# Optimization experiments

Hardware: AMD Instinct MI355X
Metric: run time of the kernel (lower is better)

Reference implementation:

```python
import jax, jax.numpy as jnp
import numpy as np

B, S, D, H = 2, 2048, 2048, 16
HD = D // H  # 128


def setup_inputs() -> dict:
    key = jax.random.key(0)
    ks = jax.random.split(key, 9)
    s = 1.0 / np.sqrt(D)
    return {
        "x": jax.random.normal(ks[0], (B, S, D), dtype=jnp.float32),
        "Wq_w": jax.random.uniform(ks[1], (D, D), jnp.float32, -s, s),
        "Wq_b": jax.random.uniform(ks[2], (D,), jnp.float32, -s, s),
        "Wk_w": jax.random.uniform(ks[3], (HD, D), jnp.float32, -s, s),
        "Wk_b": jax.random.uniform(ks[4], (HD,), jnp.float32, -s, s),
        "Wv_w": jax.random.uniform(ks[5], (HD, D), jnp.float32, -s, s),
        "Wv_b": jax.random.uniform(ks[6], (HD,), jnp.float32, -s, s),
        "Wo_w": jax.random.uniform(ks[7], (D, D), jnp.float32, -s, s),
        "Wo_b": jax.random.uniform(ks[8], (D,), jnp.float32, -s, s),
    }


def reference(x, Wq_w, Wq_b, Wk_w, Wk_b, Wv_w, Wv_b, Wo_w, Wo_b):
    b, s, d = x.shape
    h, hd = H, HD
    # projections (torch Linear: x @ W.T + b)
    q = (x @ Wq_w.T + Wq_b).reshape(b, s, h, hd).transpose(0, 2, 1, 3)  # (b,h,s,hd)
    k = x @ Wk_w.T + Wk_b  # (b,s,hd) single shared KV head
    v = x @ Wv_w.T + Wv_b  # (b,s,hd)
    scores = jnp.einsum("bhsd,btd->bhst", q, k) / jnp.sqrt(jnp.float32(hd))
    attn = jax.nn.softmax(scores, axis=-1)
    out = jnp.einsum("bhst,btd->bhsd", attn, v)  # (b,h,s,hd)
    # faithful to original: reshape WITHOUT transposing heads back
    out = out.reshape(b, s, d)
    return out @ Wo_w.T + Wo_b
```

## Files before the change

### kernel.cpp

```cpp
#include <hip/hip_runtime.h>
#include <stdint.h>

#define BATCH 2
#define SEQ   2048
#define DMOD  2048
#define NHEAD 16
#define HDIM  128

typedef __bf16 bf16x8 __attribute__((ext_vector_type(8)));
typedef float f32x4   __attribute__((ext_vector_type(4)));
typedef float f32x16  __attribute__((ext_vector_type(16)));
typedef unsigned short u16x8 __attribute__((ext_vector_type(8)));

#define MFMA16(a, b, c) __builtin_amdgcn_mfma_f32_16x16x32_bf16(a, b, c, 0, 0, 0)
#define MFMA32(a, b, c) __builtin_amdgcn_mfma_f32_32x32x16_bf16(a, b, c, 0, 0, 0)

__device__ __forceinline__ uint16_t f2bf(float f) {
  union { float f; uint32_t u; } cv; cv.f = f;
  uint32_t u = cv.u;
  return (uint16_t)((u + 0x7FFFu + ((u >> 16) & 1u)) >> 16);
}

__device__ __forceinline__ float fexp2(float x) { return exp2f(x); }

__device__ __forceinline__ uint32_t pkbf(float a, float b) {
  uint32_t d;
  asm("v_cvt_pk_bf16_f32 %0, %1, %2" : "=v"(d) : "v"(a), "v"(b));
  return d;
}

__device__ __forceinline__ void gload_lds16(const void* g, void* l) {
  __builtin_amdgcn_global_load_lds(
      (__attribute__((address_space(1))) void*)g,
      (__attribute__((address_space(3))) void*)l, 16, 0, 0);
}

__global__ __launch_bounds__(256) void cvtbf16(const float* __restrict__ in,
                                               uint16_t* __restrict__ out, int n) {
  int i = (blockIdx.x * 256 + threadIdx.x) * 8;
  if (i >= n) return;
  f32x4 a = *(const f32x4*)&in[i];
  f32x4 b = *(const f32x4*)&in[i + 4];
  u16x8 o;
  o[0] = f2bf(a[0]); o[1] = f2bf(a[1]); o[2] = f2bf(a[2]); o[3] = f2bf(a[3]);
  o[4] = f2bf(b[0]); o[5] = f2bf(b[1]); o[6] = f2bf(b[2]); o[7] = f2bf(b[3]);
  *(u16x8*)&out[i] = o;
}

template <bool OUT_F32>
__device__ __forceinline__ void gemm128_body(
    const uint16_t* __restrict__ A, int lda,
    const uint16_t* __restrict__ Bw,
    const float* __restrict__ bias,
    void* __restrict__ out, int ldc,
    int m0, int n0, int K, float oscale,
    uint16_t* As, uint16_t* Bs) {
  const int t = threadIdx.x;
  const int lane = t & 63;
  const int w = t >> 6;
  const int half = lane >> 4;
  const int fr = lane & 15;
  const int wr = w >> 1, wc = w & 1;

  f32x4 acc[4][4] = {};

  const int r0 = (0 * 4 + w) * 16 + (lane >> 2);
  const int r1 = (1 * 4 + w) * 16 + (lane >> 2);
  const int sc0 = (lane & 3) * 8;

  const int nkt = K >> 5;
  for (int kt = 0; kt < nkt; ++kt) {
    const int kb = kt * 32;
    gload_lds16(&A[(size_t)(m0 + r0) * lda + kb + sc0], &As[(0 * 4 + w) * 512]);
    gload_lds16(&A[(size_t)(m0 + r1) * lda + kb + sc0], &As[(1 * 4 + w) * 512]);
    gload_lds16(&Bw[(size_t)(n0 + r0) * K + kb + sc0], &Bs[(0 * 4 + w) * 512]);
    gload_lds16(&Bw[(size_t)(n0 + r1) * K + kb + sc0], &Bs[(1 * 4 + w) * 512]);
    __syncthreads();
    bf16x8 af[4], bf[4];
#pragma unroll
    for (int i = 0; i < 4; ++i) {
      af[i] = *(const bf16x8*)&As[(wr * 64 + i * 16 + fr) * 32 + half * 8];
      bf[i] = *(const bf16x8*)&Bs[(wc * 64 + i * 16 + fr) * 32 + half * 8];
    }
#pragma unroll
    for (int i = 0; i < 4; ++i)
#pragma unroll
      for (int j = 0; j < 4; ++j)
        acc[i][j] = MFMA16(af[i], bf[j], acc[i][j]);
    __syncthreads();
  }

#pragma unroll
  for (int j = 0; j < 4; ++j) {
    const int col = wc * 64 + j * 16 + fr;
    const float bv = bias[n0 + col];
#pragma unroll
    for (int i = 0; i < 4; ++i) {
      const int rowb = m0 + wr * 64 + i * 16 + half * 4;
#pragma unroll
      for (int r = 0; r < 4; ++r) {
        const float v = (acc[i][j][r] + bv) * oscale;
        if (OUT_F32)
          ((float*)out)[(size_t)(rowb + r) * ldc + n0 + col] = v;
        else
          ((uint16_t*)out)[(size_t)(rowb + r) * ldc + n0 + col] = f2bf(v);
      }
    }
  }
}

__global__ __launch_bounds__(256, 2) void qkv_gemm(
    const uint16_t* __restrict__ xb,
    const uint16_t* __restrict__ wqb, const float* __restrict__ bq,
    const uint16_t* __restrict__ wkb, const float* __restrict__ bk,
    const uint16_t* __restrict__ wvb, const float* __restrict__ bv,
    uint16_t* __restrict__ qb, uint16_t* __restrict__ kb, uint16_t* __restrict__ vb,
    float qscale) {
  __shared__ uint16_t As[128 * 32];
  __shared__ uint16_t Bs[128 * 32];
  const int m0 = blockIdx.x * 128;
  const int y = blockIdx.y;
  const uint16_t* Bw;
  const float* bias;
  uint16_t* out;
  int n0, ldc;
  float os = 1.0f;
  if (y < 16)       { Bw = wqb; bias = bq; out = qb; n0 = y * 128; ldc = DMOD; os = qscale; }
  else if (y == 16) { Bw = wkb; bias = bk; out = kb; n0 = 0;       ldc = HDIM; }
  else              { Bw = wvb; bias = bv; out = vb; n0 = 0;       ldc = HDIM; }
  gemm128_body<false>(xb, DMOD, Bw, bias, out, ldc, m0, n0, DMOD, os, As, Bs);
}

__global__ __launch_bounds__(256, 2) void o_gemm(
    const uint16_t* __restrict__ ab, const uint16_t* __restrict__ wob,
    const float* __restrict__ bo, float* __restrict__ out) {
  __shared__ uint16_t As[128 * 32];
  __shared__ uint16_t Bs[128 * 32];
  gemm128_body<true>(ab, DMOD, wob, bo, out, DMOD,
                     blockIdx.x * 128, blockIdx.y * 128, DMOD, 1.0f, As, Bs);
}

__global__ __launch_bounds__(256) void transpose_v(const uint16_t* __restrict__ vb,
                                                   uint16_t* __restrict__ vt) {
  __shared__ uint16_t tile[64][65];
  const int s0 = blockIdx.x * 64, d0 = blockIdx.y * 64, b = blockIdx.z;
  const int tx = threadIdx.x & 63, ty = threadIdx.x >> 6;
#pragma unroll
  for (int r = ty; r < 64; r += 4)
    tile[r][tx] = vb[((size_t)b * SEQ + s0 + r) * HDIM + d0 + tx];
  __syncthreads();
#pragma unroll
  for (int r = ty; r < 64; r += 4)
    vt[((size_t)b * HDIM + d0 + r) * SEQ + s0 + tx] = tile[tx][r];
}

__global__ __launch_bounds__(256, 2) void mqa_attn(
    const uint16_t* __restrict__ qb,
    const uint16_t* __restrict__ kb,
    const uint16_t* __restrict__ vt,
    uint16_t* __restrict__ ab) {
  __shared__ uint16_t Ks[2][64 * 128];
  __shared__ uint16_t Vs[2][128 * 64];

  const int t = threadIdx.x, lane = t & 63, w = t >> 6;
  const int l31 = lane & 31, hi = lane >> 5;
  const int qt = blockIdx.x, h = blockIdx.y, b = blockIdx.z;
  const size_t rowbase = (size_t)b * SEQ;
  const int q0 = qt * 128 + w * 32;

  bf16x8 qf[8];
  {
    const uint16_t* qrow = &qb[(rowbase + q0 + l31) * DMOD + h * HDIM + hi * 8];
#pragma unroll
    for (int c8 = 0; c8 < 8; ++c8)
      qf[c8] = *(const bf16x8*)&qrow[c8 * 16];
  }

  f32x16 ot[4] = {};
  float lsum = 0.f;

  const int skrow = lane >> 4;
  const int skcol = (lane & 15) * 8;
  const int svrow = lane >> 3;
  const int svcol = (lane & 7) * 8;

#pragma unroll
  for (int c = 0; c < 4; ++c) {
    const int ch = c * 4 + w;
    const int krow = ch * 4 + skrow;
    gload_lds16(&kb[(rowbase + krow) * HDIM + (skcol ^ ((krow & 7) << 3))],
                &Ks[0][ch * 512]);
    const int vrow = ch * 8 + svrow;
    gload_lds16(&vt[((size_t)b * HDIM + vrow) * SEQ + (svcol ^ ((vrow & 7) << 3))],
                &Vs[0][ch * 512]);
  }
  __syncthreads();

  for (int kt = 0; kt < SEQ / 64; ++kt) {
    const int cur = kt & 1;
    if (kt < SEQ / 64 - 1) {
#pragma unroll
      for (int c = 0; c < 4; ++c) {
        const int ch = c * 4 + w;
        const int krow = ch * 4 + skrow;
        gload_lds16(&kb[(rowbase + (kt + 1) * 64 + krow) * HDIM +
                        (skcol ^ ((krow & 7) << 3))],
                    &Ks[cur ^ 1][ch * 512]);
        const int vrow = ch * 8 + svrow;
        gload_lds16(&vt[((size_t)b * HDIM + vrow) * SEQ + (kt + 1) * 64 +
                        (svcol ^ ((vrow & 7) << 3))],
                    &Vs[cur ^ 1][ch * 512]);
      }
    }

    f32x16 st[2] = {};
    __builtin_amdgcn_s_setprio(1);
#pragma unroll
    for (int c8 = 0; c8 < 8; ++c8) {
#pragma unroll
      for (int tt = 0; tt < 2; ++tt) {
        const int krow = tt * 32 + l31;
        bf16x8 kf = *(const bf16x8*)&Ks[cur][krow * 128 +
                        ((c8 * 16 + hi * 8) ^ ((krow & 7) << 3))];
        st[tt] = MFMA32(kf, qf[c8], st[tt]);
      }
    }
    __builtin_amdgcn_s_setprio(0);

    uint32_t wk[2][8], rk[2][8];
    float s = 0.f;
#pragma unroll
    for (int tt = 0; tt < 2; ++tt) {
      float e[16];
#pragma unroll
      for (int i = 0; i < 16; ++i) {
        e[i] = fexp2(st[tt][i]);
        s += e[i];
      }
#pragma unroll
      for (int i = 0; i < 8; ++i)
        wk[tt][i] = pkbf(e[2 * i], e[2 * i + 1]);
    }
    s += __shfl_xor(s, 32);
    lsum += s;

#pragma unroll
    for (int tt = 0; tt < 2; ++tt)
#pragma unroll
      for (int i = 0; i < 8; ++i)
        rk[tt][i] = (uint32_t)__shfl_xor((int)wk[tt][i], 32);

    bf16x8 pf[4];
#pragma unroll
    for (int tt = 0; tt < 2; ++tt) {
      union { uint32_t u[4]; bf16x8 v; } p0, p1;
      p0.u[0] = hi ? rk[tt][2] : wk[tt][0];
      p0.u[1] = hi ? rk[tt][3] : wk[tt][1];
      p0.u[2] = hi ? wk[tt][2] : rk[tt][0];
      p0.u[3] = hi ? wk[tt][3] : rk[tt][1];
      p1.u[0] = hi ? rk[tt][6] : wk[tt][4];
      p1.u[1] = hi ? rk[tt][7] : wk[tt][5];
      p1.u[2] = hi ? wk[tt][6] : rk[tt][4];
      p1.u[3] = hi ? wk[tt][7] : rk[tt][5];
      pf[2 * tt] = p0.v;
      pf[2 * tt + 1] = p1.v;
    }

    __builtin_amdgcn_s_setprio(1);
#pragma unroll
    for (int kc = 0; kc < 4; ++kc) {
#pragma unroll
      for (int dt = 0; dt < 4; ++dt) {
        const int vrow = dt * 32 + l31;
        bf16x8 vf = *(const bf16x8*)&Vs[cur][vrow * 64 +
                        ((kc * 16 + hi * 8) ^ ((vrow & 7) << 3))];
        ot[dt] = MFMA32(vf, pf[kc], ot[dt]);
      }
    }
    __builtin_amdgcn_s_setprio(0);

    __syncthreads();
  }

  const float inv = 1.f / lsum;
  const size_t orow = ((size_t)(b * NHEAD + h) * SEQ + q0 + l31) * HDIM;
#pragma unroll
  for (int dt = 0; dt < 4; ++dt)
#pragma unroll
    for (int qd = 0; qd < 4; ++qd) {
      ushort4 hv;
      hv.x = f2bf(ot[dt][qd * 4 + 0] * inv);
      hv.y = f2bf(ot[dt][qd * 4 + 1] * inv);
      hv.z = f2bf(ot[dt][qd * 4 + 2] * inv);
      hv.w = f2bf(ot[dt][qd * 4 + 3] * inv);
      *(ushort4*)&ab[orow + dt * 32 + qd * 8 + hi * 4] = hv;
    }
}

extern "C" void kernel_launch(void* const* d_in, const int* in_sizes, int n_in,
                              void* d_out, int out_size, void* d_ws, size_t ws_size,
                              hipStream_t stream) {
  const float* x    = (const float*)d_in[0];
  const float* Wq_w = (const float*)d_in[1];
  const float* Wq_b = (const float*)d_in[2];
  const float* Wk_w = (const float*)d_in[3];
  const float* Wk_b = (const float*)d_in[4];
  const float* Wv_w = (const float*)d_in[5];
  const float* Wv_b = (const float*)d_in[6];
  const float* Wo_w = (const float*)d_in[7];
  const float* Wo_b = (const float*)d_in[8];
  float* out = (float*)d_out;

  char* ws = (char*)d_ws;
  uint16_t* xb  = (uint16_t*)(ws + 0);
  uint16_t* ab  = xb;
  uint16_t* wqb = (uint16_t*)(ws + 16777216);
  uint16_t* vt  = wqb;
  uint16_t* wkb = (uint16_t*)(ws + 25165824);
  uint16_t* wvb = (uint16_t*)(ws + 25690112);
  uint16_t* wob = (uint16_t*)(ws + 26214400);
  uint16_t* qb  = (uint16_t*)(ws + 34603008);
  uint16_t* kb  = (uint16_t*)(ws + 51380224);
  uint16_t* vb  = (uint16_t*)(ws + 52428800);

  const float qscale = 0.08838834764831845f * 1.4426950408889634f;

  cvtbf16<<<4096, 256, 0, stream>>>(x, xb, BATCH * SEQ * DMOD);
  cvtbf16<<<2048, 256, 0, stream>>>(Wq_w, wqb, DMOD * DMOD);
  cvtbf16<<<128, 256, 0, stream>>>(Wk_w, wkb, HDIM * DMOD);
  cvtbf16<<<128, 256, 0, stream>>>(Wv_w, wvb, HDIM * DMOD);
  cvtbf16<<<2048, 256, 0, stream>>>(Wo_w, wob, DMOD * DMOD);

  qkv_gemm<<<dim3(32, 18), 256, 0, stream>>>(xb, wqb, Wq_b, wkb, Wk_b, wvb, Wv_b,
                                             qb, kb, vb, qscale);
  transpose_v<<<dim3(32, 2, 2), 256, 0, stream>>>(vb, vt);
  mqa_attn<<<dim3(16, 16, 2), 256, 0, stream>>>(qb, kb, vt, ab);
  o_gemm<<<dim3(32, 16), 256, 0, stream>>>(ab, wob, Wo_b, out);
}
```

Measured before the change: 309.0 us.

## Rewrite GEMMs as 128x256 triple-buffered 8-wave kernel; use permlane32 swap in attention

Replaces the 128x128, single-stage GEMM with a 512-thread kernel that computes 128x256 tiles with K=64 steps. Loads are triple-buffered into swizzled LDS and overlapped with MFMA using explicit vmcnt waits, and tiles are mapped to XCDs for L2 locality. K and V projections are fused into one 256-wide tile alongside the Q tiles. In attention, the bf16 probability exchange between wave halves uses v_permlane32_swap instead of 16 shuffles plus selects. The larger dynamic LDS and one block per CU lower occupancy, so latency hiding relies on the pipeline.

Measured after the change: 317.2 us. +2.6%, slower.

```diff
diff --git a/kernel.cpp b/kernel.cpp
--- a/kernel.cpp
+++ b/kernel.cpp
@@ -47,97 +47,120 @@
   *(u16x8*)&out[i] = o;
 }
 
-template <bool OUT_F32>
-__device__ __forceinline__ void gemm128_body(
-    const uint16_t* __restrict__ A, int lda,
-    const uint16_t* __restrict__ Bw,
-    const float* __restrict__ bias,
-    void* __restrict__ out, int ldc,
-    int m0, int n0, int K, float oscale,
-    uint16_t* As, uint16_t* Bs) {
-  const int t = threadIdx.x;
-  const int lane = t & 63;
-  const int w = t >> 6;
-  const int half = lane >> 4;
-  const int fr = lane & 15;
-  const int wr = w >> 1, wc = w & 1;
+template <bool OUT_F32, bool HAS_KV>
+__global__ __launch_bounds__(512, 1) void gemm8(
+    const uint16_t* __restrict__ A,
+    const uint16_t* __restrict__ Bw, const float* __restrict__ bias,
+    void* __restrict__ out, int ldc, float oscale,
+    const uint16_t* __restrict__ Bkv,
+    const float* __restrict__ biask, const float* __restrict__ biasv,
+    uint16_t* __restrict__ kout, uint16_t* __restrict__ vout) {
+  extern __shared__ uint16_t smem[];
+  uint16_t* As = smem;
+  uint16_t* Bs = smem + 3 * 128 * 64;
+
+  const int lane = threadIdx.x & 63, w = threadIdx.x >> 6;
+  const int half = lane >> 4, fr = lane & 15;
+  const int wr = w >> 2, wc = w & 3;
+
+  const int f = blockIdx.x;
+  bool kvblk = false;
+  int m0, n0;
+  const uint16_t* Bb;
+  if (HAS_KV && f >= 256) {
+    kvblk = true; m0 = (f - 256) * 128; n0 = 0; Bb = Bkv;
+  } else {
+    const int xcd = f & 7, idx = f >> 3;
+    const int mblk = (xcd >> 1) * 8 + (idx & 7);
+    const int nblk = (xcd & 1) * 4 + (idx >> 3);
+    m0 = mblk * 128; n0 = nblk * 256; Bb = Bw;
+  }
+
+  const int rsub = lane >> 3;
+  const int swcol = ((lane & 7) ^ rsub) * 8;
+  const size_t a0 = (size_t)(m0 + (2 * w) * 8 + rsub) * DMOD + swcol;
+  const size_t b0 = (size_t)(n0 + (4 * w) * 8 + rsub) * DMOD + swcol;
 
   f32x4 acc[4][4] = {};
-
-  const int r0 = (0 * 4 + w) * 16 + (lane >> 2);
-  const int r1 = (1 * 4 + w) * 16 + (lane >> 2);
-  const int sc0 = (lane & 3) * 8;
-
-  const int nkt = K >> 5;
-  for (int kt = 0; kt < nkt; ++kt) {
-    const int kb = kt * 32;
-    gload_lds16(&A[(size_t)(m0 + r0) * lda + kb + sc0], &As[(0 * 4 + w) * 512]);
-    gload_lds16(&A[(size_t)(m0 + r1) * lda + kb + sc0], &As[(1 * 4 + w) * 512]);
-    gload_lds16(&Bw[(size_t)(n0 + r0) * K + kb + sc0], &Bs[(0 * 4 + w) * 512]);
-    gload_lds16(&Bw[(size_t)(n0 + r1) * K + kb + sc0], &Bs[(1 * 4 + w) * 512]);
-    __syncthreads();
-    bf16x8 af[4], bf[4];
-#pragma unroll
-    for (int i = 0; i < 4; ++i) {
-      af[i] = *(const bf16x8*)&As[(wr * 64 + i * 16 + fr) * 32 + half * 8];
-      bf[i] = *(const bf16x8*)&Bs[(wc * 64 + i * 16 + fr) * 32 + half * 8];
-    }
-#pragma unroll
-    for (int i = 0; i < 4; ++i)
+  const int NT = DMOD / 64;
+
+  auto STAGE = [&](int kt, int slot) {
+    uint16_t* Ad = As + slot * (128 * 64);
+    uint16_t* Bd = Bs + slot * (256 * 64);
+    const int kk = kt * 64;
+    gload_lds16(&A[a0 + kk],            &Ad[(2 * w) * 512]);
+    gload_lds16(&A[a0 + 8 * DMOD + kk], &Ad[(2 * w + 1) * 512]);
+    gload_lds16(&Bb[b0 + kk],             &Bd[(4 * w) * 512]);
+    gload_lds16(&Bb[b0 + 8 * DMOD + kk],  &Bd[(4 * w + 1) * 512]);
+    gload_lds16(&Bb[b0 + 16 * DMOD + kk], &Bd[(4 * w + 2) * 512]);
+    gload_lds16(&Bb[b0 + 24 * DMOD + kk], &Bd[(4 * w + 3) * 512]);
+  };
+
+  STAGE(0, 0);
+  STAGE(1, 1);
+  asm volatile("s_waitcnt vmcnt(6)" ::: "memory");
+  __builtin_amdgcn_s_barrier();
+  asm volatile("" ::: "memory");
+
+  int sc_ = 0, ss_ = 2;
+#pragma unroll 1
+  for (int t = 0; t < NT; ++t) {
+    if (t + 2 < NT) STAGE(t + 2, ss_);
+
+    const uint16_t* Ar = As + sc_ * (128 * 64);
+    const uint16_t* Br = Bs + sc_ * (256 * 64);
+#pragma unroll
+    for (int kc = 0; kc < 2; ++kc) {
+      bf16x8 af[4], bf[4];
+      const int slot = ((kc * 4 + half) ^ (fr & 7)) * 8;
+#pragma unroll
+      for (int i = 0; i < 4; ++i)
+        af[i] = *(const bf16x8*)&Ar[(wr * 64 + i * 16 + fr) * 64 + slot];
 #pragma unroll
       for (int j = 0; j < 4; ++j)
-        acc[i][j] = MFMA16(af[i], bf[j], acc[i][j]);
-    __syncthreads();
-  }
-
+        bf[j] = *(const bf16x8*)&Br[(wc * 64 + j * 16 + fr) * 64 + slot];
+      __builtin_amdgcn_s_setprio(1);
+#pragma unroll
+      for (int i = 0; i < 4; ++i)
+#pragma unroll
+        for (int j = 0; j < 4; ++j)
+          acc[i][j] = MFMA16(af[i], bf[j], acc[i][j]);
+      __builtin_amdgcn_s_setprio(0);
+    }
+
+    if (t + 2 < NT) asm volatile("s_waitcnt vmcnt(6)" ::: "memory");
+    else            asm volatile("s_waitcnt vmcnt(0)" ::: "memory");
+    if (t + 1 < NT) {
+      __builtin_amdgcn_s_barrier();
+      asm volatile("" ::: "memory");
+    }
+    sc_ = (sc_ == 2) ? 0 : sc_ + 1;
+    ss_ = (ss_ == 2) ? 0 : ss_ + 1;
+  }
+
+  const float os = kvblk ? 1.0f : oscale;
 #pragma unroll
   for (int j = 0; j < 4; ++j) {
     const int col = wc * 64 + j * 16 + fr;
-    const float bv = bias[n0 + col];
+    float bv_;
+    if (!kvblk) bv_ = bias[n0 + col];
+    else        bv_ = (col < 128) ? biask[col] : biasv[col - 128];
 #pragma unroll
     for (int i = 0; i < 4; ++i) {
       const int rowb = m0 + wr * 64 + i * 16 + half * 4;
 #pragma unroll
       for (int r = 0; r < 4; ++r) {
-        const float v = (acc[i][j][r] + bv) * oscale;
-        if (OUT_F32)
-          ((float*)out)[(size_t)(rowb + r) * ldc + n0 + col] = v;
-        else
-          ((uint16_t*)out)[(size_t)(rowb + r) * ldc + n0 + col] = f2bf(v);
-      }
-    }
-  }
-}
-
-__global__ __launch_bounds__(256, 2) void qkv_gemm(
-    const uint16_t* __restrict__ xb,
-    const uint16_t* __restrict__ wqb, const float* __restrict__ bq,
-    const uint16_t* __restrict__ wkb, const float* __restrict__ bk,
-    const uint16_t* __restrict__ wvb, const float* __restrict__ bv,
-    uint16_t* __restrict__ qb, uint16_t* __restrict__ kb, uint16_t* __restrict__ vb,
-    float qscale) {
-  __shared__ uint16_t As[128 * 32];
-  __shared__ uint16_t Bs[128 * 32];
-  const int m0 = blockIdx.x * 128;
-  const int y = blockIdx.y;
-  const uint16_t* Bw;
-  const float* bias;
-  uint16_t* out;
-  int n0, ldc;
-  float os = 1.0f;
-  if (y < 16)       { Bw = wqb; bias = bq; out = qb; n0 = y * 128; ldc = DMOD; os = qscale; }
-  else if (y == 16) { Bw = wkb; bias = bk; out = kb; n0 = 0;       ldc = HDIM; }
-  else              { Bw = wvb; bias = bv; out = vb; n0 = 0;       ldc = HDIM; }
-  gemm128_body<false>(xb, DMOD, Bw, bias, out, ldc, m0, n0, DMOD, os, As, Bs);
-}
-
-__global__ __launch_bounds__(256, 2) void o_gemm(
-    const uint16_t* __restrict__ ab, const uint16_t* __restrict__ wob,
-    const float* __restrict__ bo, float* __restrict__ out) {
-  __shared__ uint16_t As[128 * 32];
-  __shared__ uint16_t Bs[128 * 32];
-  gemm128_body<true>(ab, DMOD, wob, bo, out, DMOD,
-                     blockIdx.x * 128, blockIdx.y * 128, DMOD, 1.0f, As, Bs);
+        const float v = (acc[i][j][r] + bv_) * os;
+        if (!kvblk) {
+          if (OUT_F32) ((float*)out)[(size_t)(rowb + r) * ldc + n0 + col] = v;
+          else ((uint16_t*)out)[(size_t)(rowb + r) * ldc + n0 + col] = f2bf(v);
+        } else {
+          if (col < 128) kout[(size_t)(rowb + r) * HDIM + col] = f2bf(v);
+          else           vout[(size_t)(rowb + r) * HDIM + col - 128] = f2bf(v);
+        }
+      }
+    }
+  }
 }
 
 __global__ __launch_bounds__(256) void transpose_v(const uint16_t* __restrict__ vb,
@@ -227,7 +250,7 @@
     }
     __builtin_amdgcn_s_setprio(0);
 
-    uint32_t wk[2][8], rk[2][8];
+    uint32_t wk[2][8];
     float s = 0.f;
 #pragma unroll
     for (int tt = 0; tt < 2; ++tt) {
@@ -244,24 +267,20 @@
     s += __shfl_xor(s, 32);
     lsum += s;
 
-#pragma unroll
-    for (int tt = 0; tt < 2; ++tt)
-#pragma unroll
-      for (int i = 0; i < 8; ++i)
-        rk[tt][i] = (uint32_t)__shfl_xor((int)wk[tt][i], 32);
-
     bf16x8 pf[4];
 #pragma unroll
     for (int tt = 0; tt < 2; ++tt) {
+      uint32_t a0 = wk[tt][0], c0 = wk[tt][2];
+      uint32_t a1 = wk[tt][1], c1 = wk[tt][3];
+      uint32_t a2 = wk[tt][4], c2 = wk[tt][6];
+      uint32_t a3 = wk[tt][5], c3 = wk[tt][7];
+      asm volatile("v_permlane32_swap_b32 %0, %1" : "+v"(a0), "+v"(c0));
+      asm volatile("v_permlane32_swap_b32 %0, %1" : "+v"(a1), "+v"(c1));
+      asm volatile("v_permlane32_swap_b32 %0, %1" : "+v"(a2), "+v"(c2));
+      asm volatile("v_permlane32_swap_b32 %0, %1" : "+v"(a3), "+v"(c3));
       union { uint32_t u[4]; bf16x8 v; } p0, p1;
-      p0.u[0] = hi ? rk[tt][2] : wk[tt][0];
-      p0.u[1] = hi ? rk[tt][3] : wk[tt][1];
-      p0.u[2] = hi ? wk[tt][2] : rk[tt][0];
-      p0.u[3] = hi ? wk[tt][3] : rk[tt][1];
-      p1.u[0] = hi ? rk[tt][6] : wk[tt][4];
-      p1.u[1] = hi ? rk[tt][7] : wk[tt][5];
-      p1.u[2] = hi ? wk[tt][6] : rk[tt][4];
-      p1.u[3] = hi ? wk[tt][7] : rk[tt][5];
+      p0.u[0] = a0; p0.u[1] = a1; p0.u[2] = c0; p0.u[3] = c1;
+      p1.u[0] = a2; p1.u[1] = a3; p1.u[2] = c2; p1.u[3] = c3;
       pf[2 * tt] = p0.v;
       pf[2 * tt + 1] = p1.v;
     }
@@ -324,6 +343,12 @@
   uint16_t* vb  = (uint16_t*)(ws + 52428800);
 
   const float qscale = 0.08838834764831845f * 1.4426950408889634f;
+  const int GEMM_LDS = 3 * (128 + 256) * 64 * 2;
+
+  hipFuncSetAttribute(reinterpret_cast<const void*>(gemm8<false, true>),
+                      hipFuncAttributeMaxDynamicSharedMemorySize, GEMM_LDS);
+  hipFuncSetAttribute(reinterpret_cast<const void*>(gemm8<true, false>),
+                      hipFuncAttributeMaxDynamicSharedMemorySize, GEMM_LDS);
 
   cvtbf16<<<4096, 256, 0, stream>>>(x, xb, BATCH * SEQ * DMOD);
   cvtbf16<<<2048, 256, 0, stream>>>(Wq_w, wqb, DMOD * DMOD);
@@ -331,9 +356,10 @@
   cvtbf16<<<128, 256, 0, stream>>>(Wv_w, wvb, HDIM * DMOD);
   cvtbf16<<<2048, 256, 0, stream>>>(Wo_w, wob, DMOD * DMOD);
 
-  qkv_gemm<<<dim3(32, 18), 256, 0, stream>>>(xb, wqb, Wq_b, wkb, Wk_b, wvb, Wv_b,
-                                             qb, kb, vb, qscale);
+  gemm8<false, true><<<288, 512, GEMM_LDS, stream>>>(
+      xb, wqb, Wq_b, qb, DMOD, qscale, wkb, Wk_b, Wv_b, kb, vb);
   transpose_v<<<dim3(32, 2, 2), 256, 0, stream>>>(vb, vt);
   mqa_attn<<<dim3(16, 16, 2), 256, 0, stream>>>(qb, kb, vt, ab);
-  o_gemm<<<dim3(32, 16), 256, 0, stream>>>(ab, wob, Wo_b, out);
-}
+  gemm8<true, false><<<256, 512, GEMM_LDS, stream>>>(
+      ab, wob, Wo_b, out, DMOD, 1.0f, nullptr, nullptr, nullptr, nullptr, nullptr);
+}
```
